# Kernel tuning notes

Measured on AMD Instinct MI355X. Metric: run time of the kernel, lower is better.

The kernel has to match this reference:

```python
import jax, jax.numpy as jnp
import numpy as np

SWIGLU_ALPHA = 1.702
SWIGLU_LIMIT = 7.0

E, H, I, T = 8, 2048, 4096, 8192  # experts, hidden, intermediate, tokens


def setup_inputs() -> dict:
    key = jax.random.key(0)
    ks = jax.random.split(key, 7)
    s = 0.02
    x = jax.random.normal(ks[0], (T, H), dtype=jnp.float32)
    gate_w = jax.random.normal(ks[1], (E, H, I), dtype=jnp.float32) * s
    up_w = jax.random.normal(ks[2], (E, H, I), dtype=jnp.float32) * s
    down_w = jax.random.normal(ks[3], (E, I, H), dtype=jnp.float32) * s
    gate_b = jax.random.normal(ks[4], (E, I), dtype=jnp.float32) * s
    up_b = jax.random.normal(ks[5], (E, I), dtype=jnp.float32) * s
    down_b = jax.random.normal(ks[6], (E, H), dtype=jnp.float32) * s
    # cumulative end offsets per expert; equal contiguous groups covering all T tokens
    grouped_mm_offs = jnp.asarray(np.arange(1, E + 1) * (T // E), dtype=jnp.int32)
    return {
        "x": x,
        "grouped_mm_offs": grouped_mm_offs,
        "gate_w": gate_w,
        "up_w": up_w,
        "down_w": down_w,
        "gate_b": gate_b,
        "up_b": up_b,
        "down_b": down_b,
    }


def _grouped_mm(x, w, offs):
    """Grouped GEMM: tokens are contiguous per expert; offs are concrete end offsets."""
    starts = [0] + [int(o) for o in np.asarray(offs)]
    outs = [x[starts[e]:starts[e + 1]] @ w[e] for e in range(w.shape[0])]
    return jnp.concatenate(outs, axis=0)


def reference(x, grouped_mm_offs, gate_w, up_w, down_w, gate_b, up_b, down_b):
    n_tok = x.shape[0]
    group_ids = jnp.searchsorted(
        grouped_mm_offs.astype(jnp.int32),
        jnp.arange(n_tok, dtype=jnp.int32),
        side="right",
    )
    gate = _grouped_mm(x, gate_w, grouped_mm_offs) + gate_b[group_ids]
    up = _grouped_mm(x, up_w, grouped_mm_offs) + up_b[group_ids]
    gate = jnp.minimum(gate, SWIGLU_LIMIT)
    up = jnp.clip(up, -SWIGLU_LIMIT, SWIGLU_LIMIT)
    glu = gate * jax.nn.sigmoid(SWIGLU_ALPHA * gate)
    activated = (up + 1.0) * glu
    out = _grouped_mm(activated, down_w, grouped_mm_offs) + down_b[group_ids]
    return out
```

## Files before the change

kernel.cpp:

```cpp
#include <hip/hip_runtime.h>

typedef float  f32x4 __attribute__((ext_vector_type(4)));
typedef short  s16x8 __attribute__((ext_vector_type(8)));
typedef unsigned short u16x8 __attribute__((ext_vector_type(8)));
typedef unsigned int   u32x4 __attribute__((ext_vector_type(4)));

constexpr int E = 8, H = 2048, IDIM = 4096, T = 8192;
constexpr float ALPHA = 1.702f, LIMIT = 7.0f;

__device__ __forceinline__ unsigned short f2bf(float f) {
    unsigned int u = __builtin_bit_cast(unsigned int, f);
    u += 0x7fffu + ((u >> 16) & 1u);
    return (unsigned short)(u >> 16);
}

__device__ __forceinline__ unsigned int pk_bf16(float a, float b) {
#if __has_builtin(__builtin_amdgcn_cvt_pk_bf16_f32)
    auto v = __builtin_amdgcn_cvt_pk_bf16_f32(a, b);
    return __builtin_bit_cast(unsigned int, v);
#else
    unsigned int ua = __builtin_bit_cast(unsigned int, a);
    unsigned int ub = __builtin_bit_cast(unsigned int, b);
    ua += 0x7fffu + ((ua >> 16) & 1u);
    ub += 0x7fffu + ((ub >> 16) & 1u);
    return __builtin_amdgcn_perm(ub, ua, 0x07060302);
#endif
}

__device__ __forceinline__ f32x4 mfma16(s16x8 a, s16x8 b, f32x4 c) {
    return __builtin_amdgcn_mfma_f32_16x16x32_bf16(a, b, c, 0, 0, 0);
}

__device__ __forceinline__ int bswz(int n) { return n ^ ((n >> 2) & 7); }

__global__ __launch_bounds__(256, 2)
void gateup_kernel(const float* __restrict__ x, const int* __restrict__ offs,
                   const float* __restrict__ gate_w, const float* __restrict__ up_w,
                   const float* __restrict__ gate_b, const float* __restrict__ up_b,
                   unsigned short* __restrict__ act)
{
    __shared__ __align__(16) unsigned short As[4][128][8];
    __shared__ __align__(16) unsigned short Bg[4][128][8];
    __shared__ __align__(16) unsigned short Bu[4][128][8];

    const int tid  = threadIdx.x;
    const int row0 = blockIdx.y * 128;
    const int col0 = blockIdx.x * 128;

    int e = 0;
    while (e < E - 1 && row0 >= offs[e]) ++e;

    const float* gw = gate_w + (size_t)e * H * IDIM;
    const float* uw = up_w   + (size_t)e * H * IDIM;

    const int lane = tid & 63;
    const int wave = tid >> 6;
    const int wm   = (wave & 1) * 64;
    const int wn   = (wave >> 1) * 64;
    const int l15  = lane & 15;
    const int quad = lane >> 4;

    const int n4   = (tid & 31) * 4;
    const int grp  = tid >> 5;
    const int bsel = grp >> 2;
    const int bkb  = grp & 3;
    const float* bw = bsel ? uw : gw;
    unsigned short* brow0 = bsel ? &Bu[bkb][0][0] : &Bg[bkb][0][0];

    const f32x4 fzero = {0.f, 0.f, 0.f, 0.f};
    f32x4 accg[4][4], accu[4][4];
#pragma unroll
    for (int i = 0; i < 4; ++i)
#pragma unroll
        for (int j = 0; j < 4; ++j) { accg[i][j] = fzero; accu[i][j] = fzero; }

    for (int k0 = 0; k0 < H; k0 += 32) {
#pragma unroll
        for (int p = 0; p < 2; ++p) {
            int pair = tid + 256 * p;
            int kb = pair & 3, m = pair >> 2;
            const float* src = x + (size_t)(row0 + m) * H + k0 + kb * 8;
            f32x4 v0 = *(const f32x4*)src;
            f32x4 v1 = *(const f32x4*)(src + 4);
            u32x4 o = { pk_bf16(v0[0], v0[1]), pk_bf16(v0[2], v0[3]),
                        pk_bf16(v1[0], v1[1]), pk_bf16(v1[2], v1[3]) };
            *(u32x4*)&As[kb][m ^ (2 * kb)][0] = o;
        }
        {
            const float* src = bw + (size_t)(k0 + bkb * 8) * IDIM + col0 + n4;
            f32x4 v[8];
#pragma unroll
            for (int r = 0; r < 8; ++r) v[r] = *(const f32x4*)(src + (size_t)r * IDIM);
#pragma unroll
            for (int c = 0; c < 4; ++c) {
                u32x4 o = { pk_bf16(v[0][c], v[1][c]), pk_bf16(v[2][c], v[3][c]),
                            pk_bf16(v[4][c], v[5][c]), pk_bf16(v[6][c], v[7][c]) };
                *(u32x4*)(brow0 + (size_t)bswz(n4 + c) * 8) = o;
            }
        }
        __syncthreads();
        s16x8 afr[4], bgf[4], buf[4];
#pragma unroll
        for (int mi = 0; mi < 4; ++mi) {
            int m = wm + mi * 16 + l15;
            afr[mi] = *(const s16x8*)&As[quad][m ^ (2 * quad)][0];
        }
#pragma unroll
        for (int ni = 0; ni < 4; ++ni) {
            int n = wn + ni * 16 + l15;
            bgf[ni] = *(const s16x8*)&Bg[quad][bswz(n)][0];
            buf[ni] = *(const s16x8*)&Bu[quad][bswz(n)][0];
        }
#pragma unroll
        for (int mi = 0; mi < 4; ++mi)
#pragma unroll
            for (int ni = 0; ni < 4; ++ni) {
                accg[mi][ni] = mfma16(afr[mi], bgf[ni], accg[mi][ni]);
                accu[mi][ni] = mfma16(afr[mi], buf[ni], accu[mi][ni]);
            }
        __syncthreads();
    }

#pragma unroll
    for (int ni = 0; ni < 4; ++ni) {
        int col = col0 + wn + ni * 16 + l15;
        float gb = gate_b[(size_t)e * IDIM + col];
        float ub = up_b[(size_t)e * IDIM + col];
#pragma unroll
        for (int mi = 0; mi < 4; ++mi) {
            int rowb = row0 + wm + mi * 16 + quad * 4;
#pragma unroll
            for (int r = 0; r < 4; ++r) {
                float g = accg[mi][ni][r] + gb;
                float u = accu[mi][ni][r] + ub;
                g = fminf(g, LIMIT);
                u = fminf(fmaxf(u, -LIMIT), LIMIT);
                float glu = g / (1.0f + __expf(-ALPHA * g));
                float av  = (u + 1.0f) * glu;
                act[(size_t)(rowb + r) * IDIM + col] = f2bf(av);
            }
        }
    }
}

__global__ __launch_bounds__(256, 2)
void down_kernel(const unsigned short* __restrict__ act, const int* __restrict__ offs,
                 const float* __restrict__ down_w, const float* __restrict__ down_b,
                 float* __restrict__ out)
{
    __shared__ __align__(16) unsigned short As[8][128][8];
    __shared__ __align__(16) unsigned short Bs[8][128][8];

    const int tid  = threadIdx.x;
    const int row0 = blockIdx.y * 128;
    const int col0 = blockIdx.x * 128;

    int e = 0;
    while (e < E - 1 && row0 >= offs[e]) ++e;
    const float* dw = down_w + (size_t)e * IDIM * H;

    const int lane = tid & 63;
    const int wave = tid >> 6;
    const int wm   = (wave & 1) * 64;
    const int wn   = (wave >> 1) * 64;
    const int l15  = lane & 15;
    const int quad = lane >> 4;

    const int n4  = (tid & 31) * 4;
    const int bkb = tid >> 5;

    const f32x4 fzero = {0.f, 0.f, 0.f, 0.f};
    f32x4 acc[4][4];
#pragma unroll
    for (int i = 0; i < 4; ++i)
#pragma unroll
        for (int j = 0; j < 4; ++j) acc[i][j] = fzero;

    for (int k0 = 0; k0 < IDIM; k0 += 64) {
#pragma unroll
        for (int p = 0; p < 4; ++p) {
            int pair = tid + 256 * p;
            int kb = pair & 7, m = pair >> 3;
            *(u16x8*)&As[kb][m ^ kb][0] =
                *(const u16x8*)(act + (size_t)(row0 + m) * IDIM + k0 + kb * 8);
        }
        {
            const float* src = dw + (size_t)(k0 + bkb * 8) * H + col0 + n4;
            f32x4 v[8];
#pragma unroll
            for (int r = 0; r < 8; ++r) v[r] = *(const f32x4*)(src + (size_t)r * H);
#pragma unroll
            for (int c = 0; c < 4; ++c) {
                u32x4 o = { pk_bf16(v[0][c], v[1][c]), pk_bf16(v[2][c], v[3][c]),
                            pk_bf16(v[4][c], v[5][c]), pk_bf16(v[6][c], v[7][c]) };
                *(u32x4*)&Bs[bkb][bswz(n4 + c)][0] = o;
            }
        }
        __syncthreads();
        s16x8 a0[4], a1[4], b0[4], b1[4];
#pragma unroll
        for (int mi = 0; mi < 4; ++mi) {
            int m = wm + mi * 16 + l15;
            a0[mi] = *(const s16x8*)&As[quad    ][m ^ quad      ][0];
            a1[mi] = *(const s16x8*)&As[quad + 4][m ^ (quad + 4)][0];
        }
#pragma unroll
        for (int ni = 0; ni < 4; ++ni) {
            int n = wn + ni * 16 + l15;
            b0[ni] = *(const s16x8*)&Bs[quad    ][bswz(n)][0];
            b1[ni] = *(const s16x8*)&Bs[quad + 4][bswz(n)][0];
        }
#pragma unroll
        for (int mi = 0; mi < 4; ++mi)
#pragma unroll
            for (int ni = 0; ni < 4; ++ni) {
                acc[mi][ni] = mfma16(a0[mi], b0[ni], acc[mi][ni]);
                acc[mi][ni] = mfma16(a1[mi], b1[ni], acc[mi][ni]);
            }
        __syncthreads();
    }

#pragma unroll
    for (int ni = 0; ni < 4; ++ni) {
        int col = col0 + wn + ni * 16 + l15;
        float db = down_b[(size_t)e * H + col];
#pragma unroll
        for (int mi = 0; mi < 4; ++mi) {
            int rowb = row0 + wm + mi * 16 + quad * 4;
#pragma unroll
            for (int r = 0; r < 4; ++r)
                out[(size_t)(rowb + r) * H + col] = acc[mi][ni][r] + db;
        }
    }
}

extern "C" void kernel_launch(void* const* d_in, const int* in_sizes, int n_in,
                              void* d_out, int out_size, void* d_ws, size_t ws_size,
                              hipStream_t stream) {
    const float* x      = (const float*)d_in[0];
    const int*   offs   = (const int*)d_in[1];
    const float* gate_w = (const float*)d_in[2];
    const float* up_w   = (const float*)d_in[3];
    const float* down_w = (const float*)d_in[4];
    const float* gate_b = (const float*)d_in[5];
    const float* up_b   = (const float*)d_in[6];
    const float* down_b = (const float*)d_in[7];
    float* out = (float*)d_out;
    unsigned short* act = (unsigned short*)d_ws;

    dim3 blk(256);
    dim3 g1(IDIM / 128, T / 128);
    gateup_kernel<<<g1, blk, 0, stream>>>(x, offs, gate_w, up_w, gate_b, up_b, act);
    dim3 g2(H / 128, T / 128);
    down_kernel<<<g2, blk, 0, stream>>>(act, offs, down_w, down_b, out);
}
```

Baseline: 1.230 ms.

## Double-buffer LDS tiles with register prefetch and use 512-thread blocks

Both GEMM kernels now prefetch the next K-slice from global memory into registers while computing on the current LDS buffer, using two LDS buffers and a single barrier per step. Blocks grow to 512 threads (8 waves), each wave owning a 64x32 sub-tile, so each thread loads less and holds fewer accumulators. The aim is to hide global-load latency and halve the barriers per step, at the cost of doubled LDS footprint and possibly lower blocks per CU.

After: 1.546 ms. +25.7%, slower.

```diff
diff --git a/kernel.cpp b/kernel.cpp
--- a/kernel.cpp
+++ b/kernel.cpp
@@ -4,6 +4,7 @@
 typedef short  s16x8 __attribute__((ext_vector_type(8)));
 typedef unsigned short u16x8 __attribute__((ext_vector_type(8)));
 typedef unsigned int   u32x4 __attribute__((ext_vector_type(4)));
+typedef unsigned int   u32x2 __attribute__((ext_vector_type(2)));
 
 constexpr int E = 8, H = 2048, IDIM = 4096, T = 8192;
 constexpr float ALPHA = 1.702f, LIMIT = 7.0f;
@@ -33,15 +34,15 @@
 
 __device__ __forceinline__ int bswz(int n) { return n ^ ((n >> 2) & 7); }
 
-__global__ __launch_bounds__(256, 2)
+__global__ __launch_bounds__(512, 2)
 void gateup_kernel(const float* __restrict__ x, const int* __restrict__ offs,
                    const float* __restrict__ gate_w, const float* __restrict__ up_w,
                    const float* __restrict__ gate_b, const float* __restrict__ up_b,
                    unsigned short* __restrict__ act)
 {
-    __shared__ __align__(16) unsigned short As[4][128][8];
-    __shared__ __align__(16) unsigned short Bg[4][128][8];
-    __shared__ __align__(16) unsigned short Bu[4][128][8];
+    __shared__ __align__(16) unsigned short As[2][4][128][8];
+    __shared__ __align__(16) unsigned short Bg[2][4][128][8];
+    __shared__ __align__(16) unsigned short Bu[2][4][128][8];
 
     const int tid  = threadIdx.x;
     const int row0 = blockIdx.y * 128;
@@ -55,74 +56,87 @@
 
     const int lane = tid & 63;
     const int wave = tid >> 6;
-    const int wm   = (wave & 1) * 64;
-    const int wn   = (wave >> 1) * 64;
+    const int wm   = (wave >> 2) * 64;
+    const int wn   = (wave & 3) * 32;
     const int l15  = lane & 15;
     const int quad = lane >> 4;
 
+    const int akb = tid & 3;
+    const int am  = tid >> 2;
+    const float* asrc = x + (size_t)(row0 + am) * H + akb * 8;
+
     const int n4   = (tid & 31) * 4;
     const int grp  = tid >> 5;
-    const int bsel = grp >> 2;
-    const int bkb  = grp & 3;
+    const int bsel = grp >> 3;
+    const int bkb  = (grp >> 1) & 3;
+    const int brh  = grp & 1;
     const float* bw = bsel ? uw : gw;
-    unsigned short* brow0 = bsel ? &Bu[bkb][0][0] : &Bg[bkb][0][0];
+    const float* bsrc = bw + (size_t)(bkb * 8 + brh * 4) * IDIM + col0 + n4;
 
     const f32x4 fzero = {0.f, 0.f, 0.f, 0.f};
-    f32x4 accg[4][4], accu[4][4];
+    f32x4 accg[4][2], accu[4][2];
 #pragma unroll
     for (int i = 0; i < 4; ++i)
 #pragma unroll
-        for (int j = 0; j < 4; ++j) { accg[i][j] = fzero; accu[i][j] = fzero; }
-
-    for (int k0 = 0; k0 < H; k0 += 32) {
-#pragma unroll
-        for (int p = 0; p < 2; ++p) {
-            int pair = tid + 256 * p;
-            int kb = pair & 3, m = pair >> 2;
-            const float* src = x + (size_t)(row0 + m) * H + k0 + kb * 8;
-            f32x4 v0 = *(const f32x4*)src;
-            f32x4 v1 = *(const f32x4*)(src + 4);
-            u32x4 o = { pk_bf16(v0[0], v0[1]), pk_bf16(v0[2], v0[3]),
-                        pk_bf16(v1[0], v1[1]), pk_bf16(v1[2], v1[3]) };
-            *(u32x4*)&As[kb][m ^ (2 * kb)][0] = o;
-        }
-        {
-            const float* src = bw + (size_t)(k0 + bkb * 8) * IDIM + col0 + n4;
-            f32x4 v[8];
-#pragma unroll
-            for (int r = 0; r < 8; ++r) v[r] = *(const f32x4*)(src + (size_t)r * IDIM);
-#pragma unroll
-            for (int c = 0; c < 4; ++c) {
-                u32x4 o = { pk_bf16(v[0][c], v[1][c]), pk_bf16(v[2][c], v[3][c]),
-                            pk_bf16(v[4][c], v[5][c]), pk_bf16(v[6][c], v[7][c]) };
-                *(u32x4*)(brow0 + (size_t)bswz(n4 + c) * 8) = o;
+        for (int j = 0; j < 2; ++j) { accg[i][j] = fzero; accu[i][j] = fzero; }
+
+    f32x4 ra0, ra1, rb[4];
+
+    auto LOAD = [&](int k0) {
+        const float* s = asrc + k0;
+        ra0 = *(const f32x4*)s;
+        ra1 = *(const f32x4*)(s + 4);
+        const float* b = bsrc + (size_t)k0 * IDIM;
+#pragma unroll
+        for (int r = 0; r < 4; ++r) rb[r] = *(const f32x4*)(b + (size_t)r * IDIM);
+    };
+
+    auto STORE = [&](int buf) {
+        u32x4 o = { pk_bf16(ra0[0], ra0[1]), pk_bf16(ra0[2], ra0[3]),
+                    pk_bf16(ra1[0], ra1[1]), pk_bf16(ra1[2], ra1[3]) };
+        *(u32x4*)&As[buf][akb][am ^ (2 * akb)][0] = o;
+        unsigned short* bb = bsel ? &Bu[buf][bkb][0][0] : &Bg[buf][bkb][0][0];
+#pragma unroll
+        for (int c = 0; c < 4; ++c) {
+            u32x2 o2 = { pk_bf16(rb[0][c], rb[1][c]), pk_bf16(rb[2][c], rb[3][c]) };
+            *(u32x2*)(bb + (size_t)bswz(n4 + c) * 8 + brh * 4) = o2;
+        }
+    };
+
+    auto COMPUTE = [&](int buf) {
+        s16x8 afr[4], bgf[2], buf2[2];
+#pragma unroll
+        for (int mi = 0; mi < 4; ++mi) {
+            int m = wm + mi * 16 + l15;
+            afr[mi] = *(const s16x8*)&As[buf][quad][m ^ (2 * quad)][0];
+        }
+#pragma unroll
+        for (int ni = 0; ni < 2; ++ni) {
+            int n = wn + ni * 16 + l15;
+            bgf[ni]  = *(const s16x8*)&Bg[buf][quad][bswz(n)][0];
+            buf2[ni] = *(const s16x8*)&Bu[buf][quad][bswz(n)][0];
+        }
+#pragma unroll
+        for (int mi = 0; mi < 4; ++mi)
+#pragma unroll
+            for (int ni = 0; ni < 2; ++ni) {
+                accg[mi][ni] = mfma16(afr[mi], bgf[ni],  accg[mi][ni]);
+                accu[mi][ni] = mfma16(afr[mi], buf2[ni], accu[mi][ni]);
             }
-        }
-        __syncthreads();
-        s16x8 afr[4], bgf[4], buf[4];
-#pragma unroll
-        for (int mi = 0; mi < 4; ++mi) {
-            int m = wm + mi * 16 + l15;
-            afr[mi] = *(const s16x8*)&As[quad][m ^ (2 * quad)][0];
-        }
-#pragma unroll
-        for (int ni = 0; ni < 4; ++ni) {
-            int n = wn + ni * 16 + l15;
-            bgf[ni] = *(const s16x8*)&Bg[quad][bswz(n)][0];
-            buf[ni] = *(const s16x8*)&Bu[quad][bswz(n)][0];
-        }
-#pragma unroll
-        for (int mi = 0; mi < 4; ++mi)
-#pragma unroll
-            for (int ni = 0; ni < 4; ++ni) {
-                accg[mi][ni] = mfma16(afr[mi], bgf[ni], accg[mi][ni]);
-                accu[mi][ni] = mfma16(afr[mi], buf[ni], accu[mi][ni]);
-            }
-        __syncthreads();
-    }
-
-#pragma unroll
-    for (int ni = 0; ni < 4; ++ni) {
+    };
+
+    LOAD(0); STORE(0); __syncthreads();
+    int k = 32;
+#pragma unroll 1
+    for (int it = 0; it < 31; ++it) {
+        LOAD(k); COMPUTE(0); STORE(1); __syncthreads(); k += 32;
+        LOAD(k); COMPUTE(1); STORE(0); __syncthreads(); k += 32;
+    }
+    LOAD(k); COMPUTE(0); STORE(1); __syncthreads();
+    COMPUTE(1);
+
+#pragma unroll
+    for (int ni = 0; ni < 2; ++ni) {
         int col = col0 + wn + ni * 16 + l15;
         float gb = gate_b[(size_t)e * IDIM + col];
         float ub = up_b[(size_t)e * IDIM + col];
@@ -143,13 +157,13 @@
     }
 }
 
-__global__ __launch_bounds__(256, 2)
+__global__ __launch_bounds__(512, 2)
 void down_kernel(const unsigned short* __restrict__ act, const int* __restrict__ offs,
                  const float* __restrict__ down_w, const float* __restrict__ down_b,
                  float* __restrict__ out)
 {
-    __shared__ __align__(16) unsigned short As[8][128][8];
-    __shared__ __align__(16) unsigned short Bs[8][128][8];
+    __shared__ __align__(16) unsigned short As[2][8][128][8];
+    __shared__ __align__(16) unsigned short Bs[2][8][128][8];
 
     const int tid  = threadIdx.x;
     const int row0 = blockIdx.y * 128;
@@ -161,67 +175,85 @@
 
     const int lane = tid & 63;
     const int wave = tid >> 6;
-    const int wm   = (wave & 1) * 64;
-    const int wn   = (wave >> 1) * 64;
+    const int wm   = (wave >> 2) * 64;
+    const int wn   = (wave & 3) * 32;
     const int l15  = lane & 15;
     const int quad = lane >> 4;
 
+    const int dkb = tid & 7;
+    const int dm  = tid >> 3;
+    const unsigned short* asrc0 = act + (size_t)(row0 + dm) * IDIM + dkb * 8;
+    const unsigned short* asrc1 = act + (size_t)(row0 + dm + 64) * IDIM + dkb * 8;
+
     const int n4  = (tid & 31) * 4;
-    const int bkb = tid >> 5;
+    const int grp = tid >> 5;
+    const int bkb = grp >> 1;
+    const int brh = grp & 1;
+    const float* bsrc = dw + (size_t)(bkb * 8 + brh * 4) * H + col0 + n4;
 
     const f32x4 fzero = {0.f, 0.f, 0.f, 0.f};
-    f32x4 acc[4][4];
+    f32x4 acc[4][2];
 #pragma unroll
     for (int i = 0; i < 4; ++i)
 #pragma unroll
-        for (int j = 0; j < 4; ++j) acc[i][j] = fzero;
-
-    for (int k0 = 0; k0 < IDIM; k0 += 64) {
-#pragma unroll
-        for (int p = 0; p < 4; ++p) {
-            int pair = tid + 256 * p;
-            int kb = pair & 7, m = pair >> 3;
-            *(u16x8*)&As[kb][m ^ kb][0] =
-                *(const u16x8*)(act + (size_t)(row0 + m) * IDIM + k0 + kb * 8);
-        }
-        {
-            const float* src = dw + (size_t)(k0 + bkb * 8) * H + col0 + n4;
-            f32x4 v[8];
-#pragma unroll
-            for (int r = 0; r < 8; ++r) v[r] = *(const f32x4*)(src + (size_t)r * H);
-#pragma unroll
-            for (int c = 0; c < 4; ++c) {
-                u32x4 o = { pk_bf16(v[0][c], v[1][c]), pk_bf16(v[2][c], v[3][c]),
-                            pk_bf16(v[4][c], v[5][c]), pk_bf16(v[6][c], v[7][c]) };
-                *(u32x4*)&Bs[bkb][bswz(n4 + c)][0] = o;
-            }
-        }
-        __syncthreads();
-        s16x8 a0[4], a1[4], b0[4], b1[4];
+        for (int j = 0; j < 2; ++j) acc[i][j] = fzero;
+
+    u16x8 raA[2];
+    f32x4 rb[4];
+
+    auto LOAD = [&](int k0) {
+        raA[0] = *(const u16x8*)(asrc0 + k0);
+        raA[1] = *(const u16x8*)(asrc1 + k0);
+        const float* b = bsrc + (size_t)k0 * H;
+#pragma unroll
+        for (int r = 0; r < 4; ++r) rb[r] = *(const f32x4*)(b + (size_t)r * H);
+    };
+
+    auto STORE = [&](int buf) {
+        *(u16x8*)&As[buf][dkb][dm ^ dkb][0]        = raA[0];
+        *(u16x8*)&As[buf][dkb][(dm + 64) ^ dkb][0] = raA[1];
+#pragma unroll
+        for (int c = 0; c < 4; ++c) {
+            u32x2 o2 = { pk_bf16(rb[0][c], rb[1][c]), pk_bf16(rb[2][c], rb[3][c]) };
+            *(u32x2*)(&Bs[buf][bkb][bswz(n4 + c)][0] + brh * 4) = o2;
+        }
+    };
+
+    auto COMPUTE = [&](int buf) {
+        s16x8 a0[4], a1[4], b0[2], b1[2];
 #pragma unroll
         for (int mi = 0; mi < 4; ++mi) {
             int m = wm + mi * 16 + l15;
-            a0[mi] = *(const s16x8*)&As[quad    ][m ^ quad      ][0];
-            a1[mi] = *(const s16x8*)&As[quad + 4][m ^ (quad + 4)][0];
-        }
-#pragma unroll
-        for (int ni = 0; ni < 4; ++ni) {
+            a0[mi] = *(const s16x8*)&As[buf][quad    ][m ^ quad      ][0];
+            a1[mi] = *(const s16x8*)&As[buf][quad + 4][m ^ (quad + 4)][0];
+        }
+#pragma unroll
+        for (int ni = 0; ni < 2; ++ni) {
             int n = wn + ni * 16 + l15;
-            b0[ni] = *(const s16x8*)&Bs[quad    ][bswz(n)][0];
-            b1[ni] = *(const s16x8*)&Bs[quad + 4][bswz(n)][0];
+            b0[ni] = *(const s16x8*)&Bs[buf][quad    ][bswz(n)][0];
+            b1[ni] = *(const s16x8*)&Bs[buf][quad + 4][bswz(n)][0];
         }
 #pragma unroll
         for (int mi = 0; mi < 4; ++mi)
 #pragma unroll
-            for (int ni = 0; ni < 4; ++ni) {
+            for (int ni = 0; ni < 2; ++ni) {
                 acc[mi][ni] = mfma16(a0[mi], b0[ni], acc[mi][ni]);
                 acc[mi][ni] = mfma16(a1[mi], b1[ni], acc[mi][ni]);
             }
-        __syncthreads();
-    }
-
-#pragma unroll
-    for (int ni = 0; ni < 4; ++ni) {
+    };
+
+    LOAD(0); STORE(0); __syncthreads();
+    int k = 64;
+#pragma unroll 1
+    for (int it = 0; it < 31; ++it) {
+        LOAD(k); COMPUTE(0); STORE(1); __syncthreads(); k += 64;
+        LOAD(k); COMPUTE(1); STORE(0); __syncthreads(); k += 64;
+    }
+    LOAD(k); COMPUTE(0); STORE(1); __syncthreads();
+    COMPUTE(1);
+
+#pragma unroll
+    for (int ni = 0; ni < 2; ++ni) {
         int col = col0 + wn + ni * 16 + l15;
         float db = down_b[(size_t)e * H + col];
 #pragma unroll
@@ -248,7 +280,7 @@
     float* out = (float*)d_out;
     unsigned short* act = (unsigned short*)d_ws;
 
-    dim3 blk(256);
+    dim3 blk(512);
     dim3 g1(IDIM / 128, T / 128);
     gateup_kernel<<<g1, blk, 0, stream>>>(x, offs, gate_w, up_w, gate_b, up_b, act);
     dim3 g2(H / 128, T / 128);
```
